# Performance work log

Hardware: AMD Instinct MI355X
Metric: run time of the kernel (lower is better)

## Reference

```python
import jax, jax.numpy as jnp
import numpy as np

HEADS = 4
DIM_HEAD = 32


def setup_inputs() -> dict:
    key = jax.random.key(0)
    k1, k2, k3 = jax.random.split(key, 3)
    b, c, h, w = 2, 256, 64, 64
    hidden = HEADS * DIM_HEAD  # 128
    x = jax.random.normal(k1, (b, c, h, w), dtype=jnp.float32)
    # conv1x1 weights (out_ch, in_ch); scaled like torch default init
    w_qkv = jax.random.normal(k2, (hidden * 3, c), dtype=jnp.float32) * (1.0 / np.sqrt(c))
    w_out = jax.random.normal(k3, (c, hidden), dtype=jnp.float32) * (1.0 / np.sqrt(hidden))
    b_out = jnp.zeros((c,), dtype=jnp.float32)
    return {"x": x, "w_qkv": w_qkv, "w_out": w_out, "b_out": b_out}


def reference(x, w_qkv, w_out, b_out):
    b, c, h, w = x.shape
    hw = h * w
    scale = DIM_HEAD ** -0.5
    # 1x1 conv == channel GEMM
    qkv = jnp.einsum('oc,bchw->bohw', w_qkv, x)
    # replicate torch view(b, heads, dim_head, 3, h*w): q/k/v interleaved per channel
    qkv = qkv.reshape(b, HEADS, DIM_HEAD, 3, hw)
    q = qkv[..., 0, :] * scale           # (b, H, d, N)
    k = qkv[..., 1, :]
    v = qkv[..., 2, :]
    sim = jnp.einsum('bhdi,bhdj->bhij', q, k)   # (b, H, N, N)
    attn = jax.nn.softmax(sim, axis=-1)         # max-subtract softmax (same math)
    out = jnp.einsum('bhij,bhdj->bhid', attn, v)  # (b, H, N, d)
    out = out.transpose(0, 1, 3, 2).reshape(b, HEADS * DIM_HEAD, h, w)
    return jnp.einsum('oc,bchw->bohw', w_out, out) + b_out[None, :, None, None]
```

## Files before the change

kernel.cpp:

```cpp
#include <hip/hip_runtime.h>

#define HEADS 4
#define DIM_HEAD 32
#define NB 2
#define NC 256
#define HW 4096
#define HIDDEN 128
#define NBH (NB*HEADS)
#define ROWS_TOTAL (NBH*HW)

typedef _Float16 f16;
typedef _Float16 f16x8 __attribute__((ext_vector_type(8)));
typedef __fp16 fp16x2 __attribute__((ext_vector_type(2)));
typedef float f32x4 __attribute__((ext_vector_type(4)));

#define XT_OFF   0u
#define QT_OFF   (4u<<20)
#define KT_OFF   (6u<<20)
#define VH_OFF   (8u<<20)
#define HIDT_OFF (10u<<20)
#define WQH_OFF  (12u<<20)
#define WOH_OFF  ((12u<<20) + (256u<<10))
#define PART_OFF (13u<<20)
#define NSPLIT 3

__device__ __forceinline__ f16x8 ldg_f16x8(const f16* p) {
    union { uint4 u; f16x8 v; } t;
    t.u = *reinterpret_cast<const uint4*>(p);
    return t.v;
}
__device__ __forceinline__ unsigned packh2(float a, float b) {
    union { fp16x2 h; unsigned u; } t;
    t.h = __builtin_amdgcn_cvt_pkrtz(a, b);
    return t.u;
}

__global__ __launch_bounds__(256) void wconv(const float* __restrict__ wqkv,
                                             const float* __restrict__ wout,
                                             f16* __restrict__ wqh,
                                             f16* __restrict__ woh) {
    const int tid = blockIdx.x * 256 + threadIdx.x;
    const float QSCALE = 0.17677669529663687f * 1.4426950408889634f;
    if (tid < 24576) {
        int o_lin = tid >> 6;
        int c4 = (tid & 63) * 4;
        int which = o_lin >> 7, r = o_lin & 127;
        int head = r >> 5, d = r & 31;
        int o_g = head * 96 + d * 3 + which;
        float4 v = *reinterpret_cast<const float4*>(wqkv + o_g * 256 + c4);
        float scl = (which == 0) ? QSCALE : 1.0f;
        uint2 pv;
        pv.x = packh2(v.x * scl, v.y * scl);
        pv.y = packh2(v.z * scl, v.w * scl);
        *reinterpret_cast<uint2*>(wqh + o_lin * 256 + c4) = pv;
    } else if (tid < 24576 + 8192) {
        int t2 = tid - 24576;
        float4 v = *reinterpret_cast<const float4*>(wout + t2 * 4);
        uint2 pv;
        pv.x = packh2(v.x, v.y);
        pv.y = packh2(v.z, v.w);
        *reinterpret_cast<uint2*>(woh + t2 * 4) = pv;
    }
}

__global__ __launch_bounds__(256) void xpose(const float* __restrict__ x,
                                             f16* __restrict__ xt) {
    __shared__ float T[64][65];
    const int s0 = blockIdx.x * 64, c0 = blockIdx.y * 64, b = blockIdx.z;
    const int t = threadIdx.x;
    #pragma unroll
    for (int i = 0; i < 16; ++i) {
        int e = t + i * 256;
        int c = e >> 6, s = e & 63;
        T[c][s] = x[((size_t)(b * NC + c0 + c)) * HW + s0 + s];
    }
    __syncthreads();
    const int s = t >> 2, cg = (t & 3) * 16;
    unsigned ov[8];
    #pragma unroll
    for (int i = 0; i < 8; ++i)
        ov[i] = packh2(T[cg + 2 * i][s], T[cg + 2 * i + 1][s]);
    f16* dst = xt + ((size_t)(b * HW + s0 + s)) * 256 + c0 + cg;
    *reinterpret_cast<uint4*>(dst)     = make_uint4(ov[0], ov[1], ov[2], ov[3]);
    *reinterpret_cast<uint4*>(dst + 8) = make_uint4(ov[4], ov[5], ov[6], ov[7]);
}

__global__ __launch_bounds__(256) void qkv_mfma(const f16* __restrict__ xt,
                                                const f16* __restrict__ wqh,
                                                f16* __restrict__ qt,
                                                f16* __restrict__ kt,
                                                f16* __restrict__ vh) {
    const int w = threadIdx.x >> 6, lane = threadIdx.x & 63;
    const int q15 = lane & 15, quad = lane >> 4;
    const int b = blockIdx.z;
    const int sTile = blockIdx.x * 64 + (w & 1) * 32;
    const int oTile = blockIdx.y * 64 + (w >> 1) * 32;
    const f16* A = xt + ((size_t)(b * HW + sTile)) * 256;

    f32x4 acc[2][2];
    #pragma unroll
    for (int i = 0; i < 2; ++i)
        #pragma unroll
        for (int j = 0; j < 2; ++j) acc[i][j] = (f32x4){0.f, 0.f, 0.f, 0.f};

    #pragma unroll
    for (int kc = 0; kc < 256; kc += 32) {
        f16x8 a0 = ldg_f16x8(A + (size_t)q15 * 256 + kc + quad * 8);
        f16x8 a1 = ldg_f16x8(A + (size_t)(16 + q15) * 256 + kc + quad * 8);
        f16x8 b0 = ldg_f16x8(wqh + (size_t)(oTile + q15) * 256 + kc + quad * 8);
        f16x8 b1 = ldg_f16x8(wqh + (size_t)(oTile + 16 + q15) * 256 + kc + quad * 8);
        acc[0][0] = __builtin_amdgcn_mfma_f32_16x16x32_f16(a0, b0, acc[0][0], 0, 0, 0);
        acc[0][1] = __builtin_amdgcn_mfma_f32_16x16x32_f16(a0, b1, acc[0][1], 0, 0, 0);
        acc[1][0] = __builtin_amdgcn_mfma_f32_16x16x32_f16(a1, b0, acc[1][0], 0, 0, 0);
        acc[1][1] = __builtin_amdgcn_mfma_f32_16x16x32_f16(a1, b1, acc[1][1], 0, 0, 0);
    }

    #pragma unroll
    for (int si = 0; si < 2; ++si)
        #pragma unroll
        for (int oj = 0; oj < 2; ++oj) {
            int o_lin = oTile + oj * 16 + q15;
            int which = o_lin >> 7;
            int r = o_lin & 127;
            int head = r >> 5, d = r & 31;
            int bh = b * HEADS + head;
            int s2 = sTile + si * 16 + quad * 4;
            if (which == 2) {
                uint2 pv;
                pv.x = packh2(acc[si][oj][0], acc[si][oj][1]);
                pv.y = packh2(acc[si][oj][2], acc[si][oj][3]);
                f16* dst = vh + ((((size_t)bh * 128 + (sTile >> 5)) * 32 + d) << 5)
                              + quad * 8 + si * 4;
                *reinterpret_cast<uint2*>(dst) = pv;
            } else {
                f16* dst = (which == 0 ? qt : kt) + (size_t)bh * HW * 32;
                #pragma unroll
                for (int r2 = 0; r2 < 4; ++r2)
                    dst[(size_t)(s2 + r2) * 32 + d] = (f16)acc[si][oj][r2];
            }
        }
}

#define MFMA16(A,B,C) __builtin_amdgcn_mfma_f32_16x16x32_f16(A,B,C,0,0,0)

#define LDKV(kd0,kd1,vd0,vd1,J)                                             \
    kd0 = ldg_f16x8(Kb + (size_t)((J) + q15) * 32 + quad * 8);              \
    kd1 = ldg_f16x8(Kb + (size_t)((J) + 16 + q15) * 32 + quad * 8);         \
    vd0 = ldg_f16x8(Vb + (((size_t)((J) >> 5) * 32 + q15) << 5) + quad * 8);\
    vd1 = ldg_f16x8(Vb + (((size_t)((J) >> 5) * 32 + 16 + q15) << 5) + quad * 8);

#define CHUNK(kf0_,kf1_,vf0_,vf1_)                                       \
    {                                                                    \
        const f32x4 z = {0.f, 0.f, 0.f, 0.f};                            \
        f32x4 s0a = MFMA16(kf0_, qf0, z);                                \
        f32x4 s1a = MFMA16(kf1_, qf0, z);                                \
        f32x4 s0b = MFMA16(kf0_, qf1, z);                                \
        f32x4 s1b = MFMA16(kf1_, qf1, z);                                \
        float ea[8], eb[8];                                              \
        _Pragma("unroll")                                                \
        for (int r = 0; r < 4; ++r) {                                    \
            ea[r]   = __builtin_amdgcn_exp2f(s0a[r]);                    \
            ea[4+r] = __builtin_amdgcn_exp2f(s1a[r]);                    \
            eb[r]   = __builtin_amdgcn_exp2f(s0b[r]);                    \
            eb[4+r] = __builtin_amdgcn_exp2f(s1b[r]);                    \
        }                                                                \
        l0 += (ea[0]+ea[1])+(ea[2]+ea[3])+(ea[4]+ea[5])+(ea[6]+ea[7]);   \
        l1 += (eb[0]+eb[1])+(eb[2]+eb[3])+(eb[4]+eb[5])+(eb[6]+eb[7]);   \
        union { unsigned u[4]; f16x8 v; } pa, pb;                        \
        pa.u[0] = packh2(ea[0], ea[1]); pa.u[1] = packh2(ea[2], ea[3]);  \
        pa.u[2] = packh2(ea[4], ea[5]); pa.u[3] = packh2(ea[6], ea[7]);  \
        pb.u[0] = packh2(eb[0], eb[1]); pb.u[1] = packh2(eb[2], eb[3]);  \
        pb.u[2] = packh2(eb[4], eb[5]); pb.u[3] = packh2(eb[6], eb[7]);  \
        acc[0][0] = MFMA16(vf0_, pa.v, acc[0][0]);                       \
        acc[0][1] = MFMA16(vf1_, pa.v, acc[0][1]);                       \
        acc[1][0] = MFMA16(vf0_, pb.v, acc[1][0]);                       \
        acc[1][1] = MFMA16(vf1_, pb.v, acc[1][1]);                       \
    }

__global__ __launch_bounds__(256) void attn_mfma(const f16* __restrict__ qt,
                                                 const f16* __restrict__ kt,
                                                 const f16* __restrict__ vh,
                                                 float* __restrict__ part) {
    const int w    = threadIdx.x >> 6;
    const int lane = threadIdx.x & 63;
    const int q15  = lane & 15;
    const int quad = lane >> 4;

    const int L    = blockIdx.x;
    const int xcd  = L & 7;
    const int slot = L >> 3;
    const int combo = xcd * 3 + (slot >> 5);
    const int qblk  = slot & 31;
    const int bh    = combo & 7;
    const int split = combo >> 3;
    const int qbase = (qblk * 4 + w) * 32;

    const f16* Qb = qt + (size_t)bh * HW * 32;
    const f16* Kb = kt + (size_t)bh * HW * 32;
    const f16* Vb = vh + (size_t)bh * 128 * 1024;

    f16x8 qf0 = ldg_f16x8(Qb + (size_t)(qbase + q15) * 32 + quad * 8);
    f16x8 qf1 = ldg_f16x8(Qb + (size_t)(qbase + 16 + q15) * 32 + quad * 8);

    f32x4 acc[2][2];
    #pragma unroll
    for (int a = 0; a < 2; ++a)
        #pragma unroll
        for (int b2 = 0; b2 < 2; ++b2)
            acc[a][b2] = (f32x4){0.f, 0.f, 0.f, 0.f};
    float l0 = 0.f, l1 = 0.f;

    const int j0   = split * 1344 + (split ? 64 : 0);
    const int span = 1344 + (split == 0 ? 64 : 0);

    f16x8 ka0, ka1, va0, va1, kb0, kb1, vb0, vb1;
    LDKV(ka0, ka1, va0, va1, j0);
    LDKV(kb0, kb1, vb0, vb1, j0 + 32);

    for (int jc = 0; jc < span; jc += 64) {
        CHUNK(ka0, ka1, va0, va1);
        LDKV(ka0, ka1, va0, va1, j0 + jc + 64);
        CHUNK(kb0, kb1, vb0, vb1);
        LDKV(kb0, kb1, vb0, vb1, j0 + jc + 96);
    }

    float* P = part + (size_t)split * 33 * ROWS_TOTAL;
    #pragma unroll
    for (int qb = 0; qb < 2; ++qb) {
        float lv = qb ? l1 : l0;
        lv += __shfl_xor(lv, 16, 64);
        lv += __shfl_xor(lv, 32, 64);
        const int grow = bh * HW + qbase + qb * 16 + q15;
        if (quad == 0) P[grow] = lv;
        #pragma unroll
        for (int t = 0; t < 2; ++t)
            #pragma unroll
            for (int r = 0; r < 4; ++r) {
                int d = t * 16 + quad * 4 + r;
                P[(size_t)(1 + d) * ROWS_TOTAL + grow] = acc[qb][t][r];
            }
    }
}

__global__ __launch_bounds__(256) void attn_merge(const float* __restrict__ part,
                                                  f16* __restrict__ hidt) {
    const int t = blockIdx.x * 256 + threadIdx.x;
    const int grow = t >> 2;
    const int dq   = t & 3;
    float l = 0.f;
    #pragma unroll
    for (int sp = 0; sp < NSPLIT; ++sp)
        l += part[(size_t)sp * 33 * ROWS_TOTAL + grow];
    const float inv = 1.0f / l;
    const int bh = grow >> 12, s = grow & 4095;
    const int b = bh >> 2, h = bh & 3;

    unsigned ov[4];
    #pragma unroll
    for (int i = 0; i < 4; ++i) {
        const int d2 = dq * 4 + i;
        float o0 = 0.f, o1 = 0.f;
        #pragma unroll
        for (int sp = 0; sp < NSPLIT; ++sp) {
            const float* P = part + (size_t)sp * 33 * ROWS_TOTAL + grow;
            o0 += P[(size_t)(1 + 2 * d2) * ROWS_TOTAL];
            o1 += P[(size_t)(2 + 2 * d2) * ROWS_TOTAL];
        }
        ov[i] = packh2(o0 * inv, o1 * inv);
    }
    f16* dst = hidt + ((size_t)(b * HW + s)) * 128 + h * 32 + dq * 8;
    *reinterpret_cast<uint4*>(dst) = make_uint4(ov[0], ov[1], ov[2], ov[3]);
}

__global__ __launch_bounds__(256) void outp_mfma(const f16* __restrict__ hidt,
                                                 const f16* __restrict__ woh,
                                                 const float* __restrict__ bout,
                                                 float* __restrict__ out) {
    const int w = threadIdx.x >> 6, lane = threadIdx.x & 63;
    const int q15 = lane & 15, quad = lane >> 4;
    const int b = blockIdx.z;
    const int sTile = blockIdx.x * 64 + (w & 1) * 32;
    const int oTile = blockIdx.y * 64 + (w >> 1) * 32;
    const f16* A = hidt + ((size_t)(b * HW + sTile)) * 128;

    f32x4 acc[2][2];
    #pragma unroll
    for (int i = 0; i < 2; ++i)
        #pragma unroll
        for (int j = 0; j < 2; ++j) acc[i][j] = (f32x4){0.f, 0.f, 0.f, 0.f};

    #pragma unroll
    for (int kc = 0; kc < 128; kc += 32) {
        f16x8 a0 = ldg_f16x8(A + (size_t)q15 * 128 + kc + quad * 8);
        f16x8 a1 = ldg_f16x8(A + (size_t)(16 + q15) * 128 + kc + quad * 8);
        f16x8 b0 = ldg_f16x8(woh + (size_t)(oTile + q15) * 128 + kc + quad * 8);
        f16x8 b1 = ldg_f16x8(woh + (size_t)(oTile + 16 + q15) * 128 + kc + quad * 8);
        acc[0][0] = __builtin_amdgcn_mfma_f32_16x16x32_f16(a0, b0, acc[0][0], 0, 0, 0);
        acc[0][1] = __builtin_amdgcn_mfma_f32_16x16x32_f16(a0, b1, acc[0][1], 0, 0, 0);
        acc[1][0] = __builtin_amdgcn_mfma_f32_16x16x32_f16(a1, b0, acc[1][0], 0, 0, 0);
        acc[1][1] = __builtin_amdgcn_mfma_f32_16x16x32_f16(a1, b1, acc[1][1], 0, 0, 0);
    }

    #pragma unroll
    for (int oj = 0; oj < 2; ++oj) {
        const int o = oTile + oj * 16 + q15;
        const float bias = bout[o];
        #pragma unroll
        for (int si = 0; si < 2; ++si) {
            const int s2 = sTile + si * 16 + quad * 4;
            float4 v = make_float4(acc[si][oj][0] + bias, acc[si][oj][1] + bias,
                                   acc[si][oj][2] + bias, acc[si][oj][3] + bias);
            *reinterpret_cast<float4*>(out + ((size_t)(b * NC + o)) * HW + s2) = v;
        }
    }
}

extern "C" void kernel_launch(void* const* d_in, const int* in_sizes, int n_in,
                              void* d_out, int out_size, void* d_ws, size_t ws_size,
                              hipStream_t stream) {
    const float* x    = (const float*)d_in[0];
    const float* wqkv = (const float*)d_in[1];
    const float* wout = (const float*)d_in[2];
    const float* bout = (const float*)d_in[3];
    float* out = (float*)d_out;
    char* wsb  = (char*)d_ws;

    f16*   XT   = (f16*)(wsb + XT_OFF);
    f16*   QT   = (f16*)(wsb + QT_OFF);
    f16*   KT   = (f16*)(wsb + KT_OFF);
    f16*   VH   = (f16*)(wsb + VH_OFF);
    f16*   HIDT = (f16*)(wsb + HIDT_OFF);
    f16*   WQH  = (f16*)(wsb + WQH_OFF);
    f16*   WOH  = (f16*)(wsb + WOH_OFF);
    float* PART = (float*)(wsb + PART_OFF);

    wconv    <<<dim3(128), 256, 0, stream>>>(wqkv, wout, WQH, WOH);
    xpose    <<<dim3(64, 4, NB), 256, 0, stream>>>(x, XT);
    qkv_mfma <<<dim3(64, 6, NB), 256, 0, stream>>>(XT, WQH, QT, KT, VH);
    attn_mfma<<<dim3(768), 256, 0, stream>>>(QT, KT, VH, PART);
    attn_merge<<<dim3(512), 256, 0, stream>>>(PART, HIDT);
    outp_mfma<<<dim3(64, 4, NB), 256, 0, stream>>>(HIDT, WOH, bout, out);
}
```

Baseline: 128.4 us.

## Store GEMM operands in 16x32 fragment-tiled layout for contiguous MFMA loads

Converts the transposed input, the fp16 weights and the hidden activation buffer into a tiled layout of 16-row by 32-column blocks. Each MFMA fragment load then reads one contiguous 1 KB block instead of 16 strided rows. The attn_merge thread mapping is also changed so consecutive lanes take consecutive rows, which coalesces the partial-buffer reads. The producers and all consumers have to agree on the new indexing, which adds address arithmetic and couples the kernels.

```diff
diff --git a/kernel.cpp b/kernel.cpp
--- a/kernel.cpp
+++ b/kernel.cpp
@@ -52,14 +52,20 @@
         uint2 pv;
         pv.x = packh2(v.x * scl, v.y * scl);
         pv.y = packh2(v.z * scl, v.w * scl);
-        *reinterpret_cast<uint2*>(wqh + o_lin * 256 + c4) = pv;
+        f16* dst = wqh + (((o_lin >> 4) * 8 + (c4 >> 5)) << 9)
+                       + (o_lin & 15) * 32 + (c4 & 31);
+        *reinterpret_cast<uint2*>(dst) = pv;
     } else if (tid < 24576 + 8192) {
         int t2 = tid - 24576;
+        int o = t2 >> 5;
+        int c4 = (t2 * 4) & 127;
         float4 v = *reinterpret_cast<const float4*>(wout + t2 * 4);
         uint2 pv;
         pv.x = packh2(v.x, v.y);
         pv.y = packh2(v.z, v.w);
-        *reinterpret_cast<uint2*>(woh + t2 * 4) = pv;
+        f16* dst = woh + (((o >> 4) * 4 + (c4 >> 5)) << 9)
+                       + (o & 15) * 32 + (c4 & 31);
+        *reinterpret_cast<uint2*>(dst) = pv;
     }
 }
 
@@ -80,7 +86,9 @@
     #pragma unroll
     for (int i = 0; i < 8; ++i)
         ov[i] = packh2(T[cg + 2 * i][s], T[cg + 2 * i + 1][s]);
-    f16* dst = xt + ((size_t)(b * HW + s0 + s)) * 256 + c0 + cg;
+    const int srow = s0 + s;
+    f16* dst = xt + ((((size_t)(b * 256 + (srow >> 4))) * 8 + ((c0 + cg) >> 5)) << 9)
+                  + (srow & 15) * 32 + (cg & 31);
     *reinterpret_cast<uint4*>(dst)     = make_uint4(ov[0], ov[1], ov[2], ov[3]);
     *reinterpret_cast<uint4*>(dst + 8) = make_uint4(ov[4], ov[5], ov[6], ov[7]);
 }
@@ -95,7 +103,9 @@
     const int b = blockIdx.z;
     const int sTile = blockIdx.x * 64 + (w & 1) * 32;
     const int oTile = blockIdx.y * 64 + (w >> 1) * 32;
-    const f16* A = xt + ((size_t)(b * HW + sTile)) * 256;
+    const f16* At = xt + (((size_t)(b * 256 + (sTile >> 4))) << 12);
+    const f16* Bt = wqh + (((size_t)(oTile >> 4)) << 12);
+    const int fo = q15 * 32 + quad * 8;
 
     f32x4 acc[2][2];
     #pragma unroll
@@ -105,10 +115,11 @@
 
     #pragma unroll
     for (int kc = 0; kc < 256; kc += 32) {
-        f16x8 a0 = ldg_f16x8(A + (size_t)q15 * 256 + kc + quad * 8);
-        f16x8 a1 = ldg_f16x8(A + (size_t)(16 + q15) * 256 + kc + quad * 8);
-        f16x8 b0 = ldg_f16x8(wqh + (size_t)(oTile + q15) * 256 + kc + quad * 8);
-        f16x8 b1 = ldg_f16x8(wqh + (size_t)(oTile + 16 + q15) * 256 + kc + quad * 8);
+        const int kt5 = (kc >> 5) << 9;
+        f16x8 a0 = ldg_f16x8(At + kt5 + fo);
+        f16x8 a1 = ldg_f16x8(At + 4096 + kt5 + fo);
+        f16x8 b0 = ldg_f16x8(Bt + kt5 + fo);
+        f16x8 b1 = ldg_f16x8(Bt + 4096 + kt5 + fo);
         acc[0][0] = __builtin_amdgcn_mfma_f32_16x16x32_f16(a0, b0, acc[0][0], 0, 0, 0);
         acc[0][1] = __builtin_amdgcn_mfma_f32_16x16x32_f16(a0, b1, acc[0][1], 0, 0, 0);
         acc[1][0] = __builtin_amdgcn_mfma_f32_16x16x32_f16(a1, b0, acc[1][0], 0, 0, 0);
@@ -244,9 +255,8 @@
 
 __global__ __launch_bounds__(256) void attn_merge(const float* __restrict__ part,
                                                   f16* __restrict__ hidt) {
-    const int t = blockIdx.x * 256 + threadIdx.x;
-    const int grow = t >> 2;
-    const int dq   = t & 3;
+    const int grow = blockIdx.x * 64 + (threadIdx.x & 63);
+    const int dq   = threadIdx.x >> 6;
     float l = 0.f;
     #pragma unroll
     for (int sp = 0; sp < NSPLIT; ++sp)
@@ -268,7 +278,8 @@
         }
         ov[i] = packh2(o0 * inv, o1 * inv);
     }
-    f16* dst = hidt + ((size_t)(b * HW + s)) * 128 + h * 32 + dq * 8;
+    f16* dst = hidt + ((((size_t)(b * 256 + (s >> 4))) * 4 + h) << 9)
+                    + (s & 15) * 32 + dq * 8;
     *reinterpret_cast<uint4*>(dst) = make_uint4(ov[0], ov[1], ov[2], ov[3]);
 }
 
@@ -281,7 +292,9 @@
     const int b = blockIdx.z;
     const int sTile = blockIdx.x * 64 + (w & 1) * 32;
     const int oTile = blockIdx.y * 64 + (w >> 1) * 32;
-    const f16* A = hidt + ((size_t)(b * HW + sTile)) * 128;
+    const f16* At = hidt + (((size_t)(b * 256 + (sTile >> 4))) << 11);
+    const f16* Bt = woh + (((size_t)(oTile >> 4)) << 11);
+    const int fo = q15 * 32 + quad * 8;
 
     f32x4 acc[2][2];
     #pragma unroll
@@ -291,10 +304,11 @@
 
     #pragma unroll
     for (int kc = 0; kc < 128; kc += 32) {
-        f16x8 a0 = ldg_f16x8(A + (size_t)q15 * 128 + kc + quad * 8);
-        f16x8 a1 = ldg_f16x8(A + (size_t)(16 + q15) * 128 + kc + quad * 8);
-        f16x8 b0 = ldg_f16x8(woh + (size_t)(oTile + q15) * 128 + kc + quad * 8);
-        f16x8 b1 = ldg_f16x8(woh + (size_t)(oTile + 16 + q15) * 128 + kc + quad * 8);
+        const int kt5 = (kc >> 5) << 9;
+        f16x8 a0 = ldg_f16x8(At + kt5 + fo);
+        f16x8 a1 = ldg_f16x8(At + 2048 + kt5 + fo);
+        f16x8 b0 = ldg_f16x8(Bt + kt5 + fo);
+        f16x8 b1 = ldg_f16x8(Bt + 2048 + kt5 + fo);
         acc[0][0] = __builtin_amdgcn_mfma_f32_16x16x32_f16(a0, b0, acc[0][0], 0, 0, 0);
         acc[0][1] = __builtin_amdgcn_mfma_f32_16x16x32_f16(a0, b1, acc[0][1], 0, 0, 0);
         acc[1][0] = __builtin_amdgcn_mfma_f32_16x16x32_f16(a1, b0, acc[1][0], 0, 0, 0);
```

New measurement: 122.7 us. 4.4% less time.
